# Optimization experiments

Measured on AMD Instinct MI355X. Metric: run time of the kernel, lower is better.

The kernel has to match this reference:

```python
import jax, jax.numpy as jnp
import numpy as np

N = 100000          # num nodes
E = 1600000         # num edges
IN_F = 256
OUT_F = 256
D_LABEL = 32
ALPHA = 0.2         # LeakyReLU negative slope
EPS = 1e-9


def setup_inputs() -> dict:
    key = jax.random.key(0)
    k1, k2, k3, k4 = jax.random.split(key, 4)
    h = jax.random.normal(k1, (N, IN_F), dtype=jnp.float32)
    label = jax.random.normal(k2, (N, D_LABEL), dtype=jnp.float32)
    # xavier_uniform with gain=1.414 on [IN_F, OUT_F]
    limit = 1.414 * np.sqrt(6.0 / (IN_F + OUT_F))
    W = jax.random.uniform(k3, (IN_F, OUT_F), dtype=jnp.float32,
                           minval=-limit, maxval=limit)
    adj_indices = jax.random.randint(k4, (2, E), 0, N, dtype=jnp.int64)
    return {"h": h, "label": label, "W": W, "adj_indices": adj_indices}


def reference(h, label, W, adj_indices):
    src = adj_indices[0]  # [E]
    dst = adj_indices[1]  # [E]
    Wh = h @ W  # [N, OUT_F]
    # edge attention logits: leakyrelu(<label[src], label[dst]>)
    e = jnp.sum(label[src] * label[dst], axis=1)            # [E]
    e = jnp.where(e >= 0, e, ALPHA * e)                     # LeakyReLU
    # segment softmax over rows (src)
    exp_e = jnp.exp(e)                                      # [E]
    row_sum = jax.ops.segment_sum(exp_e, src, num_segments=N)  # [N]
    row_sum = jnp.maximum(row_sum, EPS)
    att = exp_e / row_sum[src]                              # [E]
    # dropout is identity at inference (training=False)
    # sparse-dense matmul: h_prime[i] = sum_{(i,j) in edges} att * Wh[j]
    msgs = att[:, None] * Wh[dst]                           # [E, OUT_F]
    h_prime = jax.ops.segment_sum(msgs, src, num_segments=N)  # [N, OUT_F]
    return h_prime  # concat=False -> no ELU
```

## Files before the change

### kernel.cpp

```cpp
#include <hip/hip_runtime.h>
#include <hip/hip_bf16.h>

#define NNODES 100000
#define NEDGES 1600000
#define ALPHA  0.2f
#define EPSV   1e-9f

typedef __bf16 bf16x8 __attribute__((ext_vector_type(8)));
typedef float  f32x4  __attribute__((ext_vector_type(4)));
typedef unsigned short u16x8 __attribute__((ext_vector_type(8)));

static __device__ inline unsigned short f2bf(float f) {
    unsigned int u = __float_as_uint(f);
    unsigned int r = u + 0x7fff + ((u >> 16) & 1);
    return (unsigned short)(r >> 16);
}
static __device__ inline float bf2f(unsigned short v) {
    return __uint_as_float((unsigned int)v << 16);
}

__global__ void k_zero(int* __restrict__ p, int n) {
    int i = blockIdx.x * blockDim.x + threadIdx.x;
    if (i < n) p[i] = 0;
}

__global__ void k_prepw(const float* __restrict__ W, unsigned short* __restrict__ Wt) {
    const int i = blockIdx.x * 256 + threadIdx.x;
    const int n = i >> 8, k = i & 255;
    Wt[i] = f2bf(W[k * 256 + n]);
}

#define BM 128
#define BK 32
#define LSTRIDE 40
__global__ __launch_bounds__(256, 2) void k_gemm(const float* __restrict__ h,
                                                 const unsigned short* __restrict__ Wt,
                                                 unsigned short* __restrict__ Wh) {
    __shared__ __align__(16) unsigned short As[BM * LSTRIDE];
    __shared__ __align__(16) unsigned short Bs[256 * LSTRIDE];
    const int tid  = threadIdx.x;
    const int m0   = blockIdx.x * BM;
    const int wave = tid >> 6;
    const int lane = tid & 63;
    const int wm = (wave & 1) * 64;
    const int wn = (wave >> 1) * 128;
    const int fm = lane & 15;
    const int fq = lane >> 4;
    const int fk = fq * 8;

    f32x4 acc[4][8];
    const f32x4 z = {0.f, 0.f, 0.f, 0.f};
#pragma unroll
    for (int i = 0; i < 4; ++i)
#pragma unroll
        for (int j = 0; j < 8; ++j) acc[i][j] = z;

    const int arow = tid >> 1;
    const int acol = (tid & 1) * 16;
    const bool arow_ok = (m0 + arow) < NNODES;
    const float* hrow = h + (size_t)(m0 + arow) * 256 + acol;

    for (int kc = 0; kc < 256; kc += BK) {
        float4 a0, a1, a2, a3;
        if (arow_ok) {
            a0 = *(const float4*)(hrow + kc + 0);
            a1 = *(const float4*)(hrow + kc + 4);
            a2 = *(const float4*)(hrow + kc + 8);
            a3 = *(const float4*)(hrow + kc + 12);
        } else {
            a0 = a1 = a2 = a3 = make_float4(0.f, 0.f, 0.f, 0.f);
        }
        u16x8 bv[4];
#pragma unroll
        for (int q = 0; q < 4; ++q) {
            const int c = tid + 256 * q;
            const int n = c >> 2, koff = (c & 3) * 8;
            bv[q] = *(const u16x8*)(Wt + n * 256 + kc + koff);
        }
        __syncthreads();
        u16x8 p0, p1;
        p0[0]=f2bf(a0.x); p0[1]=f2bf(a0.y); p0[2]=f2bf(a0.z); p0[3]=f2bf(a0.w);
        p0[4]=f2bf(a1.x); p0[5]=f2bf(a1.y); p0[6]=f2bf(a1.z); p0[7]=f2bf(a1.w);
        p1[0]=f2bf(a2.x); p1[1]=f2bf(a2.y); p1[2]=f2bf(a2.z); p1[3]=f2bf(a2.w);
        p1[4]=f2bf(a3.x); p1[5]=f2bf(a3.y); p1[6]=f2bf(a3.z); p1[7]=f2bf(a3.w);
        *(u16x8*)&As[arow * LSTRIDE + acol]     = p0;
        *(u16x8*)&As[arow * LSTRIDE + acol + 8] = p1;
#pragma unroll
        for (int q = 0; q < 4; ++q) {
            const int c = tid + 256 * q;
            const int n = c >> 2, koff = (c & 3) * 8;
            *(u16x8*)&Bs[n * LSTRIDE + koff] = bv[q];
        }
        __syncthreads();
        bf16x8 af[4], bfr[8];
#pragma unroll
        for (int i = 0; i < 4; ++i)
            af[i] = __builtin_bit_cast(bf16x8,
                *(const u16x8*)&As[(wm + 16 * i + fm) * LSTRIDE + fk]);
#pragma unroll
        for (int j = 0; j < 8; ++j)
            bfr[j] = __builtin_bit_cast(bf16x8,
                *(const u16x8*)&Bs[(wn + 16 * j + fm) * LSTRIDE + fk]);
#pragma unroll
        for (int i = 0; i < 4; ++i)
#pragma unroll
            for (int j = 0; j < 8; ++j)
                acc[i][j] = __builtin_amdgcn_mfma_f32_16x16x32_bf16(af[i], bfr[j], acc[i][j], 0, 0, 0);
    }
#pragma unroll
    for (int i = 0; i < 4; ++i) {
#pragma unroll
        for (int r = 0; r < 4; ++r) {
            const int grow = m0 + wm + 16 * i + fq * 4 + r;
            if (grow < NNODES) {
                unsigned short* orow = Wh + (size_t)grow * 256 + wn + fm;
#pragma unroll
                for (int j = 0; j < 8; ++j)
                    orow[16 * j] = f2bf(acc[i][j][r]);
            }
        }
    }
}

__global__ __launch_bounds__(256) void k_attn(const float* __restrict__ label,
                       const int* __restrict__ src,
                       const int* __restrict__ dst,
                       float* __restrict__ exp_e,
                       int* __restrict__ pos_in_row,
                       int* __restrict__ counts) {
    const int t = blockIdx.x * 256 + threadIdx.x;
    const int e = t >> 2;
    const int l4 = t & 3;
    if (e >= NEDGES) return;
    const int s = src[e], d = dst[e];
    const float4* ls = (const float4*)&label[s * 32 + l4 * 8];
    const float4* ld = (const float4*)&label[d * 32 + l4 * 8];
    const float4 a0 = ls[0], a1 = ls[1];
    const float4 b0 = ld[0], b1 = ld[1];
    float dot = a0.x * b0.x + a0.y * b0.y + a0.z * b0.z + a0.w * b0.w
              + a1.x * b1.x + a1.y * b1.y + a1.z * b1.z + a1.w * b1.w;
    dot += __shfl_xor(dot, 1);
    dot += __shfl_xor(dot, 2);
    if (l4 == 0) {
        const float lr = dot >= 0.f ? dot : ALPHA * dot;
        exp_e[e] = expf(lr);
        pos_in_row[e] = atomicAdd(&counts[s], 1);
    }
}

__global__ __launch_bounds__(256) void k_scan1(const int* __restrict__ counts,
                                               int* __restrict__ row_start,
                                               int* __restrict__ blockSums) {
    __shared__ int ssum[256];
    const int tid = threadIdx.x;
    const int base = blockIdx.x * 1024 + tid * 4;
    int v[4];
#pragma unroll
    for (int c = 0; c < 4; ++c) v[c] = (base + c < NNODES) ? counts[base + c] : 0;
    const int s = v[0] + v[1] + v[2] + v[3];
    ssum[tid] = s;
    __syncthreads();
    for (int off = 1; off < 256; off <<= 1) {
        const int t = (tid >= off) ? ssum[tid - off] : 0;
        __syncthreads();
        ssum[tid] += t;
        __syncthreads();
    }
    if (tid == 255) blockSums[blockIdx.x] = ssum[255];
    int p = ssum[tid] - s;
#pragma unroll
    for (int c = 0; c < 4; ++c) {
        if (base + c < NNODES) row_start[base + c] = p;
        p += v[c];
    }
}

__global__ __launch_bounds__(256) void k_scan2(int* __restrict__ blockSums, int nb) {
    __shared__ int ssum[256];
    const int tid = threadIdx.x;
    const int s = (tid < nb) ? blockSums[tid] : 0;
    ssum[tid] = s;
    __syncthreads();
    for (int off = 1; off < 256; off <<= 1) {
        const int t = (tid >= off) ? ssum[tid - off] : 0;
        __syncthreads();
        ssum[tid] += t;
        __syncthreads();
    }
    if (tid < nb) blockSums[tid] = ssum[tid] - s;
}

__global__ void k_scan3(int* __restrict__ row_start, const int* __restrict__ blockSums) {
    const int i = blockIdx.x * blockDim.x + threadIdx.x;
    if (i < NNODES) row_start[i] += blockSums[i >> 10];
}

__global__ void k_scatter(const int* __restrict__ src,
                          const int* __restrict__ dst,
                          const float* __restrict__ exp_e,
                          const int* __restrict__ pos_in_row,
                          const int* __restrict__ row_start,
                          uint2* __restrict__ sorted_pack) {
    const int e = blockIdx.x * blockDim.x + threadIdx.x;
    if (e >= NEDGES) return;
    const int pos = row_start[src[e]] + pos_in_row[e];
    sorted_pack[pos] = make_uint2((unsigned)dst[e], __float_as_uint(exp_e[e]));
}

__global__ __launch_bounds__(256) void k_aggregate(const unsigned short* __restrict__ Wh,
                                                   const int* __restrict__ row_start,
                                                   const uint2* __restrict__ sorted_pack,
                                                   float* __restrict__ out) {
    const int node = blockIdx.x * 8 + (threadIdx.x >> 5);
    if (node >= NNODES) return;
    const int sub = threadIdx.x & 31;
    const int rs = row_start[node];
    const int re = (node == NNODES - 1) ? NEDGES : row_start[node + 1];
    const unsigned short* __restrict__ Whc = Wh + sub * 8;
    float acc[8] = {0.f, 0.f, 0.f, 0.f, 0.f, 0.f, 0.f, 0.f};
    float wsum = 0.f;
    int i = rs;
    for (; i + 4 <= re; i += 4) {
        const uint2 p0 = sorted_pack[i + 0];
        const uint2 p1 = sorted_pack[i + 1];
        const uint2 p2 = sorted_pack[i + 2];
        const uint2 p3 = sorted_pack[i + 3];
        const u16x8 v0 = *(const u16x8*)&Whc[(size_t)p0.x * 256];
        const u16x8 v1 = *(const u16x8*)&Whc[(size_t)p1.x * 256];
        const u16x8 v2 = *(const u16x8*)&Whc[(size_t)p2.x * 256];
        const u16x8 v3 = *(const u16x8*)&Whc[(size_t)p3.x * 256];
        const float w0 = __uint_as_float(p0.y), w1 = __uint_as_float(p1.y);
        const float w2 = __uint_as_float(p2.y), w3 = __uint_as_float(p3.y);
        wsum += (w0 + w1) + (w2 + w3);
#pragma unroll
        for (int c = 0; c < 8; ++c) {
            acc[c] = fmaf(w0, bf2f(v0[c]), acc[c]);
            acc[c] = fmaf(w1, bf2f(v1[c]), acc[c]);
            acc[c] = fmaf(w2, bf2f(v2[c]), acc[c]);
            acc[c] = fmaf(w3, bf2f(v3[c]), acc[c]);
        }
    }
    for (; i < re; ++i) {
        const uint2 p = sorted_pack[i];
        const u16x8 v = *(const u16x8*)&Whc[(size_t)p.x * 256];
        const float w = __uint_as_float(p.y);
        wsum += w;
#pragma unroll
        for (int c = 0; c < 8; ++c) acc[c] = fmaf(w, bf2f(v[c]), acc[c]);
    }
    const float inv = 1.f / fmaxf(wsum, EPSV);
    float4 o0 = make_float4(acc[0] * inv, acc[1] * inv, acc[2] * inv, acc[3] * inv);
    float4 o1 = make_float4(acc[4] * inv, acc[5] * inv, acc[6] * inv, acc[7] * inv);
    float* orow = out + (size_t)node * 256 + sub * 8;
    *(float4*)(orow + 0) = o0;
    *(float4*)(orow + 4) = o1;
}

extern "C" void kernel_launch(void* const* d_in, const int* in_sizes, int n_in,
                              void* d_out, int out_size, void* d_ws, size_t ws_size,
                              hipStream_t stream) {
    const float* h     = (const float*)d_in[0];
    const float* label = (const float*)d_in[1];
    const float* W     = (const float*)d_in[2];
    const int*   adj   = (const int*)d_in[3];
    const int* src = adj;
    const int* dst = adj + NEDGES;
    float* out = (float*)d_out;

    char* ws = (char*)d_ws;
    unsigned short* Wh  = (unsigned short*)(ws + 0);
    unsigned short* Wt  = (unsigned short*)(ws + 51200000);
    float* exp_e        = (float*)(ws + 51400000);
    int*   pos_in_row   = (int*)  (ws + 57800000);
    uint2* sorted_pack  = (uint2*)(ws + 64200000);
    int*   counts       = (int*)  (ws + 77000000);
    int*   row_start    = (int*)  (ws + 77400000);
    int*   blockSums    = (int*)  (ws + 77800000);

    k_zero<<<(NNODES + 255) / 256, 256, 0, stream>>>(counts, NNODES);
    k_prepw<<<256, 256, 0, stream>>>(W, Wt);
    k_gemm<<<(NNODES + BM - 1) / BM, 256, 0, stream>>>(h, Wt, Wh);
    k_attn<<<(4 * NEDGES + 255) / 256, 256, 0, stream>>>(label, src, dst, exp_e, pos_in_row, counts);

    const int nb = (NNODES + 1023) / 1024;
    k_scan1<<<nb, 256, 0, stream>>>(counts, row_start, blockSums);
    k_scan2<<<1, 256, 0, stream>>>(blockSums, nb);
    k_scan3<<<(NNODES + 255) / 256, 256, 0, stream>>>(row_start, blockSums);

    k_scatter<<<(NEDGES + 255) / 256, 256, 0, stream>>>(src, dst, exp_e, pos_in_row,
                                                        row_start, sorted_pack);
    k_aggregate<<<(NNODES + 7) / 8, 256, 0, stream>>>(Wh, row_start, sorted_pack, out);
}
```

Baseline: 427.1 us.

## Split edge counting from attention, fuse scatter with attention, prefetch gathers in aggregate

Edge counting now runs in its own light kernel before the scan. Attention logit computation is fused with the CSR scatter through a per-row cursor filled by atomics, which removes the exp_e and pos_in_row intermediate arrays and the separate scatter pass. The aggregate kernel gains a software pipeline that prefetches the packed edge entries two groups ahead and the Wh rows one group ahead, to hide gather latency. The cost is more register use, and the order of edges inside a row is no longer deterministic.

```diff
diff --git a/kernel.cpp b/kernel.cpp
--- a/kernel.cpp
+++ b/kernel.cpp
@@ -122,12 +122,70 @@
     }
 }
 
-__global__ __launch_bounds__(256) void k_attn(const float* __restrict__ label,
-                       const int* __restrict__ src,
-                       const int* __restrict__ dst,
-                       float* __restrict__ exp_e,
-                       int* __restrict__ pos_in_row,
-                       int* __restrict__ counts) {
+__global__ __launch_bounds__(256) void k_count(const int* __restrict__ src,
+                                               int* __restrict__ counts) {
+    const int e = blockIdx.x * 256 + threadIdx.x;
+    if (e < NEDGES) atomicAdd(&counts[src[e]], 1);
+}
+
+__global__ __launch_bounds__(256) void k_scan1(const int* __restrict__ counts,
+                                               int* __restrict__ row_start,
+                                               int* __restrict__ blockSums) {
+    __shared__ int ssum[256];
+    const int tid = threadIdx.x;
+    const int base = blockIdx.x * 1024 + tid * 4;
+    int v[4];
+#pragma unroll
+    for (int c = 0; c < 4; ++c) v[c] = (base + c < NNODES) ? counts[base + c] : 0;
+    const int s = v[0] + v[1] + v[2] + v[3];
+    ssum[tid] = s;
+    __syncthreads();
+    for (int off = 1; off < 256; off <<= 1) {
+        const int t = (tid >= off) ? ssum[tid - off] : 0;
+        __syncthreads();
+        ssum[tid] += t;
+        __syncthreads();
+    }
+    if (tid == 255) blockSums[blockIdx.x] = ssum[255];
+    int p = ssum[tid] - s;
+#pragma unroll
+    for (int c = 0; c < 4; ++c) {
+        if (base + c < NNODES) row_start[base + c] = p;
+        p += v[c];
+    }
+}
+
+__global__ __launch_bounds__(256) void k_scan2(int* __restrict__ blockSums, int nb) {
+    __shared__ int ssum[256];
+    const int tid = threadIdx.x;
+    const int s = (tid < nb) ? blockSums[tid] : 0;
+    ssum[tid] = s;
+    __syncthreads();
+    for (int off = 1; off < 256; off <<= 1) {
+        const int t = (tid >= off) ? ssum[tid - off] : 0;
+        __syncthreads();
+        ssum[tid] += t;
+        __syncthreads();
+    }
+    if (tid < nb) blockSums[tid] = ssum[tid] - s;
+}
+
+__global__ void k_scan3(int* __restrict__ row_start,
+                        int* __restrict__ cursor,
+                        const int* __restrict__ blockSums) {
+    const int i = blockIdx.x * blockDim.x + threadIdx.x;
+    if (i < NNODES) {
+        const int v = row_start[i] + blockSums[i >> 10];
+        row_start[i] = v;
+        cursor[i] = v;
+    }
+}
+
+__global__ __launch_bounds__(256) void k_attn_scatter(const float* __restrict__ label,
+                                                      const int* __restrict__ src,
+                                                      const int* __restrict__ dst,
+                                                      int* __restrict__ cursor,
+                                                      uint2* __restrict__ sorted_pack) {
     const int t = blockIdx.x * 256 + threadIdx.x;
     const int e = t >> 2;
     const int l4 = t & 3;
@@ -143,68 +201,27 @@
     dot += __shfl_xor(dot, 2);
     if (l4 == 0) {
         const float lr = dot >= 0.f ? dot : ALPHA * dot;
-        exp_e[e] = expf(lr);
-        pos_in_row[e] = atomicAdd(&counts[s], 1);
-    }
-}
-
-__global__ __launch_bounds__(256) void k_scan1(const int* __restrict__ counts,
-                                               int* __restrict__ row_start,
-                                               int* __restrict__ blockSums) {
-    __shared__ int ssum[256];
-    const int tid = threadIdx.x;
-    const int base = blockIdx.x * 1024 + tid * 4;
-    int v[4];
-#pragma unroll
-    for (int c = 0; c < 4; ++c) v[c] = (base + c < NNODES) ? counts[base + c] : 0;
-    const int s = v[0] + v[1] + v[2] + v[3];
-    ssum[tid] = s;
-    __syncthreads();
-    for (int off = 1; off < 256; off <<= 1) {
-        const int t = (tid >= off) ? ssum[tid - off] : 0;
-        __syncthreads();
-        ssum[tid] += t;
-        __syncthreads();
-    }
-    if (tid == 255) blockSums[blockIdx.x] = ssum[255];
-    int p = ssum[tid] - s;
-#pragma unroll
-    for (int c = 0; c < 4; ++c) {
-        if (base + c < NNODES) row_start[base + c] = p;
-        p += v[c];
-    }
-}
-
-__global__ __launch_bounds__(256) void k_scan2(int* __restrict__ blockSums, int nb) {
-    __shared__ int ssum[256];
-    const int tid = threadIdx.x;
-    const int s = (tid < nb) ? blockSums[tid] : 0;
-    ssum[tid] = s;
-    __syncthreads();
-    for (int off = 1; off < 256; off <<= 1) {
-        const int t = (tid >= off) ? ssum[tid - off] : 0;
-        __syncthreads();
-        ssum[tid] += t;
-        __syncthreads();
-    }
-    if (tid < nb) blockSums[tid] = ssum[tid] - s;
-}
-
-__global__ void k_scan3(int* __restrict__ row_start, const int* __restrict__ blockSums) {
-    const int i = blockIdx.x * blockDim.x + threadIdx.x;
-    if (i < NNODES) row_start[i] += blockSums[i >> 10];
-}
-
-__global__ void k_scatter(const int* __restrict__ src,
-                          const int* __restrict__ dst,
-                          const float* __restrict__ exp_e,
-                          const int* __restrict__ pos_in_row,
-                          const int* __restrict__ row_start,
-                          uint2* __restrict__ sorted_pack) {
-    const int e = blockIdx.x * blockDim.x + threadIdx.x;
-    if (e >= NEDGES) return;
-    const int pos = row_start[src[e]] + pos_in_row[e];
-    sorted_pack[pos] = make_uint2((unsigned)dst[e], __float_as_uint(exp_e[e]));
+        const float ee = expf(lr);
+        const int pos = atomicAdd(&cursor[s], 1);
+        sorted_pack[pos] = make_uint2((unsigned)d, __float_as_uint(ee));
+    }
+}
+
+static __device__ inline void consume4(const uint2 pa, const uint2 pb,
+                                       const uint2 pc, const uint2 pd,
+                                       const u16x8 va, const u16x8 vb,
+                                       const u16x8 vc, const u16x8 vd,
+                                       float acc[8], float& wsum) {
+    const float w0 = __uint_as_float(pa.y), w1 = __uint_as_float(pb.y);
+    const float w2 = __uint_as_float(pc.y), w3 = __uint_as_float(pd.y);
+    wsum += (w0 + w1) + (w2 + w3);
+#pragma unroll
+    for (int c = 0; c < 8; ++c) {
+        acc[c] = fmaf(w0, bf2f(va[c]), acc[c]);
+        acc[c] = fmaf(w1, bf2f(vb[c]), acc[c]);
+        acc[c] = fmaf(w2, bf2f(vc[c]), acc[c]);
+        acc[c] = fmaf(w3, bf2f(vd[c]), acc[c]);
+    }
 }
 
 __global__ __launch_bounds__(256) void k_aggregate(const unsigned short* __restrict__ Wh,
@@ -220,25 +237,50 @@
     float acc[8] = {0.f, 0.f, 0.f, 0.f, 0.f, 0.f, 0.f, 0.f};
     float wsum = 0.f;
     int i = rs;
-    for (; i + 4 <= re; i += 4) {
-        const uint2 p0 = sorted_pack[i + 0];
-        const uint2 p1 = sorted_pack[i + 1];
-        const uint2 p2 = sorted_pack[i + 2];
-        const uint2 p3 = sorted_pack[i + 3];
-        const u16x8 v0 = *(const u16x8*)&Whc[(size_t)p0.x * 256];
-        const u16x8 v1 = *(const u16x8*)&Whc[(size_t)p1.x * 256];
-        const u16x8 v2 = *(const u16x8*)&Whc[(size_t)p2.x * 256];
-        const u16x8 v3 = *(const u16x8*)&Whc[(size_t)p3.x * 256];
-        const float w0 = __uint_as_float(p0.y), w1 = __uint_as_float(p1.y);
-        const float w2 = __uint_as_float(p2.y), w3 = __uint_as_float(p3.y);
-        wsum += (w0 + w1) + (w2 + w3);
-#pragma unroll
-        for (int c = 0; c < 8; ++c) {
-            acc[c] = fmaf(w0, bf2f(v0[c]), acc[c]);
-            acc[c] = fmaf(w1, bf2f(v1[c]), acc[c]);
-            acc[c] = fmaf(w2, bf2f(v2[c]), acc[c]);
-            acc[c] = fmaf(w3, bf2f(v3[c]), acc[c]);
-        }
+
+    uint2 P0 = make_uint2(0u, 0u), P1 = P0, P2 = P0, P3 = P0;
+    uint2 Q0 = P0, Q1 = P0, Q2 = P0, Q3 = P0;
+    u16x8 V0{}, V1{}, V2{}, V3{};
+
+    if (i + 4 <= re) {
+        P0 = sorted_pack[i + 0]; P1 = sorted_pack[i + 1];
+        P2 = sorted_pack[i + 2]; P3 = sorted_pack[i + 3];
+    }
+    if (i + 8 <= re) {
+        Q0 = sorted_pack[i + 4]; Q1 = sorted_pack[i + 5];
+        Q2 = sorted_pack[i + 6]; Q3 = sorted_pack[i + 7];
+    }
+    if (i + 4 <= re) {
+        V0 = *(const u16x8*)&Whc[(size_t)P0.x * 256];
+        V1 = *(const u16x8*)&Whc[(size_t)P1.x * 256];
+        V2 = *(const u16x8*)&Whc[(size_t)P2.x * 256];
+        V3 = *(const u16x8*)&Whc[(size_t)P3.x * 256];
+    }
+    for (; i + 12 <= re; i += 4) {
+        const uint2 R0 = sorted_pack[i + 8],  R1 = sorted_pack[i + 9];
+        const uint2 R2 = sorted_pack[i + 10], R3 = sorted_pack[i + 11];
+        const u16x8 W0 = *(const u16x8*)&Whc[(size_t)Q0.x * 256];
+        const u16x8 W1 = *(const u16x8*)&Whc[(size_t)Q1.x * 256];
+        const u16x8 W2 = *(const u16x8*)&Whc[(size_t)Q2.x * 256];
+        const u16x8 W3 = *(const u16x8*)&Whc[(size_t)Q3.x * 256];
+        consume4(P0, P1, P2, P3, V0, V1, V2, V3, acc, wsum);
+        P0 = Q0; P1 = Q1; P2 = Q2; P3 = Q3;
+        Q0 = R0; Q1 = R1; Q2 = R2; Q3 = R3;
+        V0 = W0; V1 = W1; V2 = W2; V3 = W3;
+    }
+    if (i + 8 <= re) {
+        const u16x8 W0 = *(const u16x8*)&Whc[(size_t)Q0.x * 256];
+        const u16x8 W1 = *(const u16x8*)&Whc[(size_t)Q1.x * 256];
+        const u16x8 W2 = *(const u16x8*)&Whc[(size_t)Q2.x * 256];
+        const u16x8 W3 = *(const u16x8*)&Whc[(size_t)Q3.x * 256];
+        consume4(P0, P1, P2, P3, V0, V1, V2, V3, acc, wsum);
+        P0 = Q0; P1 = Q1; P2 = Q2; P3 = Q3;
+        V0 = W0; V1 = W1; V2 = W2; V3 = W3;
+        i += 4;
+    }
+    if (i + 4 <= re) {
+        consume4(P0, P1, P2, P3, V0, V1, V2, V3, acc, wsum);
+        i += 4;
     }
     for (; i < re; ++i) {
         const uint2 p = sorted_pack[i];
@@ -270,8 +312,7 @@
     char* ws = (char*)d_ws;
     unsigned short* Wh  = (unsigned short*)(ws + 0);
     unsigned short* Wt  = (unsigned short*)(ws + 51200000);
-    float* exp_e        = (float*)(ws + 51400000);
-    int*   pos_in_row   = (int*)  (ws + 57800000);
+    int*   cursor       = (int*)  (ws + 57800000);
     uint2* sorted_pack  = (uint2*)(ws + 64200000);
     int*   counts       = (int*)  (ws + 77000000);
     int*   row_start    = (int*)  (ws + 77400000);
@@ -280,14 +321,14 @@
     k_zero<<<(NNODES + 255) / 256, 256, 0, stream>>>(counts, NNODES);
     k_prepw<<<256, 256, 0, stream>>>(W, Wt);
     k_gemm<<<(NNODES + BM - 1) / BM, 256, 0, stream>>>(h, Wt, Wh);
-    k_attn<<<(4 * NEDGES + 255) / 256, 256, 0, stream>>>(label, src, dst, exp_e, pos_in_row, counts);
+    k_count<<<(NEDGES + 255) / 256, 256, 0, stream>>>(src, counts);
 
     const int nb = (NNODES + 1023) / 1024;
     k_scan1<<<nb, 256, 0, stream>>>(counts, row_start, blockSums);
     k_scan2<<<1, 256, 0, stream>>>(blockSums, nb);
-    k_scan3<<<(NNODES + 255) / 256, 256, 0, stream>>>(row_start, blockSums);
-
-    k_scatter<<<(NEDGES + 255) / 256, 256, 0, stream>>>(src, dst, exp_e, pos_in_row,
-                                                        row_start, sorted_pack);
+    k_scan3<<<(NNODES + 255) / 256, 256, 0, stream>>>(row_start, cursor, blockSums);
+
+    k_attn_scatter<<<(4 * NEDGES + 255) / 256, 256, 0, stream>>>(label, src, dst,
+                                                                 cursor, sorted_pack);
     k_aggregate<<<(NNODES + 7) / 8, 256, 0, stream>>>(Wh, row_start, sorted_pack, out);
 }
```

Result: slower. 485.2 us (+13.6%).

## Fuse edge attention computation into aggregation and simplify CSR build

Applied to the files above, without the earlier changes.

Removes the separate edge-attention kernel. Attention logits are now recomputed inside the aggregation kernel from label rows, with 8 lanes per edge doing the dot product and shuffles broadcasting the weights. The CSR build now only counts degrees and scatters dst indices through an atomic cursor, which drops the exp_e and pos_in_row arrays and shrinks the sorted payload from 8 to 4 bytes per edge. In exchange the aggregation kernel does extra gathers of label[dst], and atomic cursor ordering makes summation order within a row nondeterministic.

```diff
diff --git a/kernel.cpp b/kernel.cpp
--- a/kernel.cpp
+++ b/kernel.cpp
@@ -122,30 +122,10 @@
     }
 }
 
-__global__ __launch_bounds__(256) void k_attn(const float* __restrict__ label,
-                       const int* __restrict__ src,
-                       const int* __restrict__ dst,
-                       float* __restrict__ exp_e,
-                       int* __restrict__ pos_in_row,
-                       int* __restrict__ counts) {
-    const int t = blockIdx.x * 256 + threadIdx.x;
-    const int e = t >> 2;
-    const int l4 = t & 3;
-    if (e >= NEDGES) return;
-    const int s = src[e], d = dst[e];
-    const float4* ls = (const float4*)&label[s * 32 + l4 * 8];
-    const float4* ld = (const float4*)&label[d * 32 + l4 * 8];
-    const float4 a0 = ls[0], a1 = ls[1];
-    const float4 b0 = ld[0], b1 = ld[1];
-    float dot = a0.x * b0.x + a0.y * b0.y + a0.z * b0.z + a0.w * b0.w
-              + a1.x * b1.x + a1.y * b1.y + a1.z * b1.z + a1.w * b1.w;
-    dot += __shfl_xor(dot, 1);
-    dot += __shfl_xor(dot, 2);
-    if (l4 == 0) {
-        const float lr = dot >= 0.f ? dot : ALPHA * dot;
-        exp_e[e] = expf(lr);
-        pos_in_row[e] = atomicAdd(&counts[s], 1);
-    }
+__global__ __launch_bounds__(256) void k_count(const int* __restrict__ src,
+                                               int* __restrict__ counts) {
+    const int e = blockIdx.x * 256 + threadIdx.x;
+    if (e < NEDGES) atomicAdd(&counts[src[e]], 1);
 }
 
 __global__ __launch_bounds__(256) void k_scan1(const int* __restrict__ counts,
@@ -190,47 +170,69 @@
     if (tid < nb) blockSums[tid] = ssum[tid] - s;
 }
 
-__global__ void k_scan3(int* __restrict__ row_start, const int* __restrict__ blockSums) {
+__global__ void k_scan3(int* __restrict__ row_start,
+                        int* __restrict__ cursor,
+                        const int* __restrict__ blockSums) {
     const int i = blockIdx.x * blockDim.x + threadIdx.x;
-    if (i < NNODES) row_start[i] += blockSums[i >> 10];
-}
-
-__global__ void k_scatter(const int* __restrict__ src,
-                          const int* __restrict__ dst,
-                          const float* __restrict__ exp_e,
-                          const int* __restrict__ pos_in_row,
-                          const int* __restrict__ row_start,
-                          uint2* __restrict__ sorted_pack) {
-    const int e = blockIdx.x * blockDim.x + threadIdx.x;
+    if (i < NNODES) {
+        const int v = row_start[i] + blockSums[i >> 10];
+        row_start[i] = v;
+        cursor[i] = v;
+    }
+}
+
+__global__ __launch_bounds__(256) void k_scatter(const int* __restrict__ src,
+                                                 const int* __restrict__ dst,
+                                                 int* __restrict__ cursor,
+                                                 int* __restrict__ sorted_dst) {
+    const int e = blockIdx.x * 256 + threadIdx.x;
     if (e >= NEDGES) return;
-    const int pos = row_start[src[e]] + pos_in_row[e];
-    sorted_pack[pos] = make_uint2((unsigned)dst[e], __float_as_uint(exp_e[e]));
+    const int pos = atomicAdd(&cursor[src[e]], 1);
+    sorted_dst[pos] = dst[e];
 }
 
 __global__ __launch_bounds__(256) void k_aggregate(const unsigned short* __restrict__ Wh,
+                                                   const float* __restrict__ label,
                                                    const int* __restrict__ row_start,
-                                                   const uint2* __restrict__ sorted_pack,
+                                                   const int* __restrict__ sorted_dst,
                                                    float* __restrict__ out) {
     const int node = blockIdx.x * 8 + (threadIdx.x >> 5);
     if (node >= NNODES) return;
-    const int sub = threadIdx.x & 31;
+    const int lane = threadIdx.x & 63;
+    const int sub  = lane & 31;
+    const int base32 = lane & 32;
+    const int g  = sub >> 3;
+    const int c4 = (sub & 7) * 4;
     const int rs = row_start[node];
     const int re = (node == NNODES - 1) ? NEDGES : row_start[node + 1];
     const unsigned short* __restrict__ Whc = Wh + sub * 8;
+
+    const float4 lsv = *(const float4*)&label[(size_t)node * 32 + c4];
+
     float acc[8] = {0.f, 0.f, 0.f, 0.f, 0.f, 0.f, 0.f, 0.f};
     float wsum = 0.f;
     int i = rs;
     for (; i + 4 <= re; i += 4) {
-        const uint2 p0 = sorted_pack[i + 0];
-        const uint2 p1 = sorted_pack[i + 1];
-        const uint2 p2 = sorted_pack[i + 2];
-        const uint2 p3 = sorted_pack[i + 3];
-        const u16x8 v0 = *(const u16x8*)&Whc[(size_t)p0.x * 256];
-        const u16x8 v1 = *(const u16x8*)&Whc[(size_t)p1.x * 256];
-        const u16x8 v2 = *(const u16x8*)&Whc[(size_t)p2.x * 256];
-        const u16x8 v3 = *(const u16x8*)&Whc[(size_t)p3.x * 256];
-        const float w0 = __uint_as_float(p0.y), w1 = __uint_as_float(p1.y);
-        const float w2 = __uint_as_float(p2.y), w3 = __uint_as_float(p3.y);
+        const int d0 = sorted_dst[i + 0];
+        const int d1 = sorted_dst[i + 1];
+        const int d2 = sorted_dst[i + 2];
+        const int d3 = sorted_dst[i + 3];
+        const int dm = (g & 2) ? ((g & 1) ? d3 : d2) : ((g & 1) ? d1 : d0);
+        const float4 ldv = *(const float4*)&label[(size_t)dm * 32 + c4];
+        const u16x8 v0 = *(const u16x8*)&Whc[(size_t)d0 * 256];
+        const u16x8 v1 = *(const u16x8*)&Whc[(size_t)d1 * 256];
+        const u16x8 v2 = *(const u16x8*)&Whc[(size_t)d2 * 256];
+        const u16x8 v3 = *(const u16x8*)&Whc[(size_t)d3 * 256];
+        float p = lsv.x * ldv.x + lsv.y * ldv.y + lsv.z * ldv.z + lsv.w * ldv.w;
+        p += __shfl_xor(p, 1);
+        p += __shfl_xor(p, 2);
+        p += __shfl_xor(p, 4);
+        const float lr = fmaxf(p, ALPHA * p);
+        const float wv = expf(lr);
+        const float w0 = __shfl(wv, base32 + 0);
+        const float w1 = __shfl(wv, base32 + 8);
+        const float w2 = __shfl(wv, base32 + 16);
+        const float w3 = __shfl(wv, base32 + 24);
         wsum += (w0 + w1) + (w2 + w3);
 #pragma unroll
         for (int c = 0; c < 8; ++c) {
@@ -241,9 +243,15 @@
         }
     }
     for (; i < re; ++i) {
-        const uint2 p = sorted_pack[i];
-        const u16x8 v = *(const u16x8*)&Whc[(size_t)p.x * 256];
-        const float w = __uint_as_float(p.y);
+        const int d = sorted_dst[i];
+        const float4 ldv = *(const float4*)&label[(size_t)d * 32 + c4];
+        const u16x8 v = *(const u16x8*)&Whc[(size_t)d * 256];
+        float p = lsv.x * ldv.x + lsv.y * ldv.y + lsv.z * ldv.z + lsv.w * ldv.w;
+        p += __shfl_xor(p, 1);
+        p += __shfl_xor(p, 2);
+        p += __shfl_xor(p, 4);
+        const float lr = fmaxf(p, ALPHA * p);
+        const float w = expf(lr);
         wsum += w;
 #pragma unroll
         for (int c = 0; c < 8; ++c) acc[c] = fmaf(w, bf2f(v[c]), acc[c]);
@@ -270,24 +278,22 @@
     char* ws = (char*)d_ws;
     unsigned short* Wh  = (unsigned short*)(ws + 0);
     unsigned short* Wt  = (unsigned short*)(ws + 51200000);
-    float* exp_e        = (float*)(ws + 51400000);
-    int*   pos_in_row   = (int*)  (ws + 57800000);
-    uint2* sorted_pack  = (uint2*)(ws + 64200000);
-    int*   counts       = (int*)  (ws + 77000000);
-    int*   row_start    = (int*)  (ws + 77400000);
-    int*   blockSums    = (int*)  (ws + 77800000);
+    int* sorted_dst     = (int*)  (ws + 51400000);
+    int* counts         = (int*)  (ws + 57800000);
+    int* row_start      = (int*)  (ws + 58200000);
+    int* cursor         = (int*)  (ws + 58600000);
+    int* blockSums      = (int*)  (ws + 59000000);
 
     k_zero<<<(NNODES + 255) / 256, 256, 0, stream>>>(counts, NNODES);
     k_prepw<<<256, 256, 0, stream>>>(W, Wt);
     k_gemm<<<(NNODES + BM - 1) / BM, 256, 0, stream>>>(h, Wt, Wh);
-    k_attn<<<(4 * NEDGES + 255) / 256, 256, 0, stream>>>(label, src, dst, exp_e, pos_in_row, counts);
+    k_count<<<(NEDGES + 255) / 256, 256, 0, stream>>>(src, counts);
 
     const int nb = (NNODES + 1023) / 1024;
     k_scan1<<<nb, 256, 0, stream>>>(counts, row_start, blockSums);
     k_scan2<<<1, 256, 0, stream>>>(blockSums, nb);
-    k_scan3<<<(NNODES + 255) / 256, 256, 0, stream>>>(row_start, blockSums);
-
-    k_scatter<<<(NEDGES + 255) / 256, 256, 0, stream>>>(src, dst, exp_e, pos_in_row,
-                                                        row_start, sorted_pack);
-    k_aggregate<<<(NNODES + 7) / 8, 256, 0, stream>>>(Wh, row_start, sorted_pack, out);
-}
+    k_scan3<<<(NNODES + 255) / 256, 256, 0, stream>>>(row_start, cursor, blockSums);
+
+    k_scatter<<<(NEDGES + 255) / 256, 256, 0, stream>>>(src, dst, cursor, sorted_dst);
+    k_aggregate<<<(NNODES + 7) / 8, 256, 0, stream>>>(Wh, label, row_start, sorted_dst, out);
+}
```

Measured after the change: 545.4 us. 1.28x slower.

## Fuse GEMM with attention-logit pass and fold scan fixup into consumers

Applied to the files above, without the earlier changes.

Merges the zeroing and weight-transpose kernels into one init kernel. Combines the dense GEMM and the per-edge attention/count kernel into a single launch, interleaving one GEMM block with 32 attention blocks so the memory-bound gather work overlaps the matrix work. Drops the third scan pass by having scatter and aggregate add the block prefix offsets themselves. This removes three launches and one pass over row_start, at the cost of extra blockSums reads and a fused kernel whose register and LDS footprint is sized for the GEMM, which may limit occupancy for the attention blocks.

```diff
diff --git a/kernel.cpp b/kernel.cpp
--- a/kernel.cpp
+++ b/kernel.cpp
@@ -19,27 +19,63 @@
     return __uint_as_float((unsigned int)v << 16);
 }
 
-__global__ void k_zero(int* __restrict__ p, int n) {
-    int i = blockIdx.x * blockDim.x + threadIdx.x;
-    if (i < n) p[i] = 0;
-}
-
-__global__ void k_prepw(const float* __restrict__ W, unsigned short* __restrict__ Wt) {
+__global__ void k_init(const float* __restrict__ W, unsigned short* __restrict__ Wt,
+                       int* __restrict__ counts) {
     const int i = blockIdx.x * 256 + threadIdx.x;
-    const int n = i >> 8, k = i & 255;
-    Wt[i] = f2bf(W[k * 256 + n]);
+    if (i < NNODES) counts[i] = 0;
+    if (i < 65536) {
+        const int n = i >> 8, k = i & 255;
+        Wt[i] = f2bf(W[k * 256 + n]);
+    }
 }
 
 #define BM 128
 #define BK 32
 #define LSTRIDE 40
-__global__ __launch_bounds__(256, 2) void k_gemm(const float* __restrict__ h,
-                                                 const unsigned short* __restrict__ Wt,
-                                                 unsigned short* __restrict__ Wh) {
+#define GEMM_BLOCKS 782
+#define ATTN_BLOCKS 25000
+
+__global__ __launch_bounds__(256, 2) void k_gemm_attn(const float* __restrict__ h,
+                                                      const unsigned short* __restrict__ Wt,
+                                                      unsigned short* __restrict__ Wh,
+                                                      const float* __restrict__ label,
+                                                      const int* __restrict__ src,
+                                                      const int* __restrict__ dst,
+                                                      float* __restrict__ exp_e,
+                                                      int* __restrict__ pos_in_row,
+                                                      int* __restrict__ counts) {
     __shared__ __align__(16) unsigned short As[BM * LSTRIDE];
     __shared__ __align__(16) unsigned short Bs[256 * LSTRIDE];
-    const int tid  = threadIdx.x;
-    const int m0   = blockIdx.x * BM;
+    const int tid = threadIdx.x;
+    const int bid = blockIdx.x;
+    const int q = bid / 33;
+    const int r = bid - q * 33;
+
+    if (r != 0) {
+        const int aid = q * 32 + (r - 1);
+        if (aid >= ATTN_BLOCKS) return;
+        const int t = aid * 256 + tid;
+        const int e = t >> 2;
+        const int l4 = t & 3;
+        if (e >= NEDGES) return;
+        const int s = src[e], d = dst[e];
+        const float4* ls = (const float4*)&label[s * 32 + l4 * 8];
+        const float4* ld = (const float4*)&label[d * 32 + l4 * 8];
+        const float4 a0 = ls[0], a1 = ls[1];
+        const float4 b0 = ld[0], b1 = ld[1];
+        float dot = a0.x * b0.x + a0.y * b0.y + a0.z * b0.z + a0.w * b0.w
+                  + a1.x * b1.x + a1.y * b1.y + a1.z * b1.z + a1.w * b1.w;
+        dot += __shfl_xor(dot, 1);
+        dot += __shfl_xor(dot, 2);
+        if (l4 == 0) {
+            const float lr = dot >= 0.f ? dot : ALPHA * dot;
+            exp_e[e] = expf(lr);
+            pos_in_row[e] = atomicAdd(&counts[s], 1);
+        }
+        return;
+    }
+
+    const int m0   = q * BM;
     const int wave = tid >> 6;
     const int lane = tid & 63;
     const int wm = (wave & 1) * 64;
@@ -72,10 +108,10 @@
         }
         u16x8 bv[4];
 #pragma unroll
-        for (int q = 0; q < 4; ++q) {
-            const int c = tid + 256 * q;
+        for (int qq = 0; qq < 4; ++qq) {
+            const int c = tid + 256 * qq;
             const int n = c >> 2, koff = (c & 3) * 8;
-            bv[q] = *(const u16x8*)(Wt + n * 256 + kc + koff);
+            bv[qq] = *(const u16x8*)(Wt + n * 256 + kc + koff);
         }
         __syncthreads();
         u16x8 p0, p1;
@@ -86,10 +122,10 @@
         *(u16x8*)&As[arow * LSTRIDE + acol]     = p0;
         *(u16x8*)&As[arow * LSTRIDE + acol + 8] = p1;
 #pragma unroll
-        for (int q = 0; q < 4; ++q) {
-            const int c = tid + 256 * q;
+        for (int qq = 0; qq < 4; ++qq) {
+            const int c = tid + 256 * qq;
             const int n = c >> 2, koff = (c & 3) * 8;
-            *(u16x8*)&Bs[n * LSTRIDE + koff] = bv[q];
+            *(u16x8*)&Bs[n * LSTRIDE + koff] = bv[qq];
         }
         __syncthreads();
         bf16x8 af[4], bfr[8];
@@ -110,41 +146,15 @@
 #pragma unroll
     for (int i = 0; i < 4; ++i) {
 #pragma unroll
-        for (int r = 0; r < 4; ++r) {
-            const int grow = m0 + wm + 16 * i + fq * 4 + r;
+        for (int rr = 0; rr < 4; ++rr) {
+            const int grow = m0 + wm + 16 * i + fq * 4 + rr;
             if (grow < NNODES) {
                 unsigned short* orow = Wh + (size_t)grow * 256 + wn + fm;
 #pragma unroll
                 for (int j = 0; j < 8; ++j)
-                    orow[16 * j] = f2bf(acc[i][j][r]);
+                    orow[16 * j] = f2bf(acc[i][j][rr]);
             }
         }
-    }
-}
-
-__global__ __launch_bounds__(256) void k_attn(const float* __restrict__ label,
-                       const int* __restrict__ src,
-                       const int* __restrict__ dst,
-                       float* __restrict__ exp_e,
-                       int* __restrict__ pos_in_row,
-                       int* __restrict__ counts) {
-    const int t = blockIdx.x * 256 + threadIdx.x;
-    const int e = t >> 2;
-    const int l4 = t & 3;
-    if (e >= NEDGES) return;
-    const int s = src[e], d = dst[e];
-    const float4* ls = (const float4*)&label[s * 32 + l4 * 8];
-    const float4* ld = (const float4*)&label[d * 32 + l4 * 8];
-    const float4 a0 = ls[0], a1 = ls[1];
-    const float4 b0 = ld[0], b1 = ld[1];
-    float dot = a0.x * b0.x + a0.y * b0.y + a0.z * b0.z + a0.w * b0.w
-              + a1.x * b1.x + a1.y * b1.y + a1.z * b1.z + a1.w * b1.w;
-    dot += __shfl_xor(dot, 1);
-    dot += __shfl_xor(dot, 2);
-    if (l4 == 0) {
-        const float lr = dot >= 0.f ? dot : ALPHA * dot;
-        exp_e[e] = expf(lr);
-        pos_in_row[e] = atomicAdd(&counts[s], 1);
     }
 }
 
@@ -190,32 +200,31 @@
     if (tid < nb) blockSums[tid] = ssum[tid] - s;
 }
 
-__global__ void k_scan3(int* __restrict__ row_start, const int* __restrict__ blockSums) {
-    const int i = blockIdx.x * blockDim.x + threadIdx.x;
-    if (i < NNODES) row_start[i] += blockSums[i >> 10];
-}
-
-__global__ void k_scatter(const int* __restrict__ src,
-                          const int* __restrict__ dst,
-                          const float* __restrict__ exp_e,
-                          const int* __restrict__ pos_in_row,
-                          const int* __restrict__ row_start,
-                          uint2* __restrict__ sorted_pack) {
-    const int e = blockIdx.x * blockDim.x + threadIdx.x;
+__global__ __launch_bounds__(256) void k_scatter(const int* __restrict__ src,
+                                                 const int* __restrict__ dst,
+                                                 const float* __restrict__ exp_e,
+                                                 const int* __restrict__ pos_in_row,
+                                                 const int* __restrict__ row_start,
+                                                 const int* __restrict__ blockSums,
+                                                 uint2* __restrict__ sorted_pack) {
+    const int e = blockIdx.x * 256 + threadIdx.x;
     if (e >= NEDGES) return;
-    const int pos = row_start[src[e]] + pos_in_row[e];
+    const int s = src[e];
+    const int pos = row_start[s] + blockSums[s >> 10] + pos_in_row[e];
     sorted_pack[pos] = make_uint2((unsigned)dst[e], __float_as_uint(exp_e[e]));
 }
 
 __global__ __launch_bounds__(256) void k_aggregate(const unsigned short* __restrict__ Wh,
                                                    const int* __restrict__ row_start,
+                                                   const int* __restrict__ blockSums,
                                                    const uint2* __restrict__ sorted_pack,
                                                    float* __restrict__ out) {
     const int node = blockIdx.x * 8 + (threadIdx.x >> 5);
     if (node >= NNODES) return;
     const int sub = threadIdx.x & 31;
-    const int rs = row_start[node];
-    const int re = (node == NNODES - 1) ? NEDGES : row_start[node + 1];
+    const int rs = row_start[node] + blockSums[node >> 10];
+    const int re = (node == NNODES - 1) ? NEDGES
+                                        : row_start[node + 1] + blockSums[(node + 1) >> 10];
     const unsigned short* __restrict__ Whc = Wh + sub * 8;
     float acc[8] = {0.f, 0.f, 0.f, 0.f, 0.f, 0.f, 0.f, 0.f};
     float wsum = 0.f;
@@ -277,17 +286,19 @@
     int*   row_start    = (int*)  (ws + 77400000);
     int*   blockSums    = (int*)  (ws + 77800000);
 
-    k_zero<<<(NNODES + 255) / 256, 256, 0, stream>>>(counts, NNODES);
-    k_prepw<<<256, 256, 0, stream>>>(W, Wt);
-    k_gemm<<<(NNODES + BM - 1) / BM, 256, 0, stream>>>(h, Wt, Wh);
-    k_attn<<<(4 * NEDGES + 255) / 256, 256, 0, stream>>>(label, src, dst, exp_e, pos_in_row, counts);
+    k_init<<<(65536 + 255) / 256 > (NNODES + 255) / 256 ? (65536 + 255) / 256
+                                                        : (NNODES + 255) / 256,
+             256, 0, stream>>>(W, Wt, counts);
+
+    k_gemm_attn<<<GEMM_BLOCKS * 33, 256, 0, stream>>>(h, Wt, Wh, label, src, dst,
+                                                      exp_e, pos_in_row, counts);
 
     const int nb = (NNODES + 1023) / 1024;
     k_scan1<<<nb, 256, 0, stream>>>(counts, row_start, blockSums);
     k_scan2<<<1, 256, 0, stream>>>(blockSums, nb);
-    k_scan3<<<(NNODES + 255) / 256, 256, 0, stream>>>(row_start, blockSums);
 
     k_scatter<<<(NEDGES + 255) / 256, 256, 0, stream>>>(src, dst, exp_e, pos_in_row,
-                                                        row_start, sorted_pack);
-    k_aggregate<<<(NNODES + 7) / 8, 256, 0, stream>>>(Wh, row_start, sorted_pack, out);
-}
+                                                        row_start, blockSums, sorted_pack);
+    k_aggregate<<<(NNODES + 7) / 8, 256, 0, stream>>>(Wh, row_start, blockSums,
+                                                      sorted_pack, out);
+}
```

Result: slower. 467.5 us (+9.5%).
